# Kernel optimization log

Measured on AMD Instinct MI355X. Metric: run time of the kernel, lower is better.

Reference implementation:

```python
import jax, jax.numpy as jnp
import numpy as np

V = 32000   # vocab
H = 512     # hidden = embed dim
L = 2       # lstm layers
S = 64      # source length
K = 3       # beam width
T = 50      # max decode length
BOS = 1


def lstm_cell(x, h, c, Wih, Whh, b):
    # x,h,c: [B,H]; Wih/Whh: [4H,H]; b: [4H]
    z = x @ Wih.T + h @ Whh.T + b
    i, f, g, o = jnp.split(z, 4, axis=-1)
    c = jax.nn.sigmoid(f) * c + jax.nn.sigmoid(i) * jnp.tanh(g)
    h = jax.nn.sigmoid(o) * jnp.tanh(c)
    return h, c


def run_layer(x, Wih, Whh, b):
    # x: [S,B,H] -> outputs [S,B,H], final h,c [B,H]
    B = x.shape[1]
    z = jnp.zeros((B, H), x.dtype)
    def step(carry, xt):
        h, c = carry
        h, c = lstm_cell(xt, h, c, Wih, Whh, b)
        return (h, c), h
    (h, c), ys = jax.lax.scan(step, (z, z), x)
    return ys, h, c


def setup_inputs() -> dict:
    key = jax.random.key(0)
    ks = jax.random.split(key, 10)
    def p(k, shape, s=0.05):
        return jax.random.normal(k, shape, dtype=jnp.float32) * s
    return {
        'input_seq': jax.random.randint(ks[0], (S, 1), 0, V),
        'emb_enc': p(ks[1], (V, H), 0.1),
        'Wih_enc': p(ks[2], (L, 4 * H, H)),
        'Whh_enc': p(ks[3], (L, 4 * H, H)),
        'b_enc': jnp.zeros((L, 4 * H), jnp.float32),
        'emb_dec': p(ks[4], (V, H), 0.1),
        'Wih_dec': p(ks[5], (L, 4 * H, H)),
        'Whh_dec': p(ks[6], (L, 4 * H, H)),
        'b_dec': jnp.zeros((L, 4 * H), jnp.float32),
        'W_c': p(ks[7], (H, 2 * H)),
        'W_out': p(ks[8], (V, H)),
        'b_out': jnp.zeros((V,), jnp.float32),
        'input_length': S,
        'max_length': T,
        'bos': BOS,
    }


def reference(input_seq, emb_enc, Wih_enc, Whh_enc, b_enc,
              emb_dec, Wih_dec, Whh_dec, b_dec, W_c, W_out, b_out,
              input_length, max_length, bos):
    # ---- encoder ----
    x = emb_enc[input_seq[:, 0]][:, None, :]        # [S,1,H]
    hs, cs = [], []
    for l in range(L):
        x, hl, cl = run_layer(x, Wih_enc[l], Whh_enc[l], b_enc[l])
        hs.append(hl); cs.append(cl)
    enc_out = x[:, 0, :]                            # [S,H]
    h = jnp.stack(hs)                               # [L,1,H]
    c = jnp.stack(cs)

    # ---- decoder single step (vectorized over beam) ----
    def decode_step(tokens, h, c):
        x = emb_dec[tokens]                         # [B,H]
        nh, nc = [], []
        for l in range(L):
            hl, cl = lstm_cell(x, h[l], c[l], Wih_dec[l], Whh_dec[l], b_dec[l])
            nh.append(hl); nc.append(cl); x = hl
        attn = jax.nn.softmax(jnp.einsum('sh,bh->bs', enc_out, x), axis=-1)
        ctx = attn @ enc_out                        # [B,H]
        feat = jnp.tanh(jnp.concatenate([x, ctx], -1) @ W_c.T)
        probs = jax.nn.softmax(feat @ W_out.T + b_out)  # [B,V]
        return probs, jnp.stack(nh), jnp.stack(nc)

    # ---- first step (beam expand) ----
    probs, h, c = decode_step(jnp.array([bos]), h, c)
    topv, topi = jax.lax.top_k(probs[0], K)
    scores = jnp.log(topv)                          # [K]
    tokens = topi                                   # [K]
    h = jnp.repeat(h, K, axis=1)                    # [L,K,H]
    c = jnp.repeat(c, K, axis=1)
    backtrack = jnp.full((K, max_length), bos, dtype=jnp.int32)

    # ---- beam search loop ----
    def body(carry, t):
        tokens, h, c, scores, bt = carry
        probs, hn, cn = decode_step(tokens, h, c)   # [K,V]
        topv, topi = jax.lax.top_k(probs, K)        # [K,K]
        cum = jnp.log(topv) + scores[:, None]
        cand_scores, flat = jax.lax.top_k(cum.reshape(-1), K)
        best = topi.reshape(-1)[flat]
        orig = flat // K                            # beam origins
        bt = bt[orig].at[:, t + 1].set(tokens[orig])
        return (best, hn[:, orig, :], cn[:, orig, :], cand_scores, bt), None

    (tokens, h, c, scores, backtrack), _ = jax.lax.scan(
        body, (tokens, h, c, scores, backtrack), jnp.arange(max_length - 1))
    return backtrack[jnp.argmax(scores)]            # [max_length] tokens
```

## Files before the change

kernel.cpp:

```cpp
#include <hip/hip_runtime.h>
#include <math.h>

#define HSZ   512
#define H4    2048
#define SEQ   64
#define VOC   32000
#define BEAM  3
#define TMAX  50
#define FLS   16

#define LOFF  ((size_t)H4 * HSZ)

__device__ __forceinline__ float wsum(float v) {
#pragma unroll
  for (int off = 32; off; off >>= 1) v += __shfl_xor(v, off, 64);
  return v;
}
__device__ __forceinline__ float dot4(float4 a, float4 b) {
  return a.x * b.x + a.y * b.y + a.z * b.z + a.w * b.w;
}
__device__ __forceinline__ float sigf(float x) { return 1.f / (1.f + expf(-x)); }

__device__ __forceinline__ bool better(float v1, int i1, float v2, int i2) {
  return (v1 > v2) || (v1 == v2 && i1 < i2);
}
__device__ __forceinline__ void ins3(float* v, int* idx, float nv, int ni) {
  if (better(nv, ni, v[2], idx[2])) {
    if (better(nv, ni, v[1], idx[1])) {
      v[2] = v[1]; idx[2] = idx[1];
      if (better(nv, ni, v[0], idx[0])) { v[1] = v[0]; idx[1] = idx[0]; v[0] = nv; idx[0] = ni; }
      else { v[1] = nv; idx[1] = ni; }
    } else { v[2] = nv; idx[2] = ni; }
  }
}

__device__ __forceinline__ float agld(const float* p) {
  return __hip_atomic_load(p, __ATOMIC_RELAXED, __HIP_MEMORY_SCOPE_AGENT);
}
__device__ __forceinline__ void agst(float* p, float v) {
  __hip_atomic_store(p, v, __ATOMIC_RELAXED, __HIP_MEMORY_SCOPE_AGENT);
}
__device__ __forceinline__ int agldi(const int* p) {
  return __hip_atomic_load(p, __ATOMIC_RELAXED, __HIP_MEMORY_SCOPE_AGENT);
}


__global__ void __launch_bounds__(512) k_xw1(const float* __restrict__ Wih,
                                             const float* __restrict__ bias,
                                             const float* __restrict__ emb,
                                             const int* __restrict__ seq,
                                             float* __restrict__ xp1) {
  int t    = threadIdx.x & 63;
  int wave = threadIdx.x >> 6;
  int r    = blockIdx.x * 8 + wave;
  int tok  = seq[t];
  const float* xr = emb + (size_t)tok * HSZ;
  const float* wr = Wih + (size_t)r * HSZ;
  float acc = 0.f;
  for (int e = 0; e < HSZ; e += 4) {
    float4 wv = *(const float4*)(wr + e);
    float4 xv = *(const float4*)(xr + e);
    acc += dot4(wv, xv);
  }
  xp1[t * H4 + r] = acc + bias[r];
}

__global__ void __launch_bounds__(512) k_encslot(const float* __restrict__ Whh1,
                                                 const float* __restrict__ Wih2,
                                                 const float* __restrict__ Whh2,
                                                 const float* __restrict__ b2,
                                                 const float* __restrict__ xp1,
                                                 float* __restrict__ h1a, float* __restrict__ c1a,
                                                 float* __restrict__ h2a, float* __restrict__ c2a,
                                                 int s) {
  __shared__ float rowX[HSZ], rowH[HSZ], zl[16];
  int tid = threadIdx.x, wave = tid >> 6, lane = tid & 63;
  bool l2 = blockIdx.x >= 128;
  int t = l2 ? s - 1 : s;
  if (t < 0 || t >= SEQ) return;
  int bb = blockIdx.x & 127;
  int lr = wave >> 1;
  int j  = bb * 4 + lr;
  int g0 = (wave & 1) * 2;
  if (!l2) {
    rowX[tid] = (t > 0) ? h1a[t * HSZ + tid] : 0.f;
    __syncthreads();
    float4 h0 = ((const float4*)rowX)[lane], h1v = ((const float4*)rowX)[lane + 64];
#pragma unroll
    for (int gg = 0; gg < 2; ++gg) {
      int g = g0 + gg;
      int row = j + (g << 9);
      const float4* wr = (const float4*)(Whh1 + (size_t)row * HSZ);
      float zs = wsum(dot4(wr[lane], h0) + dot4(wr[lane + 64], h1v));
      if (lane == 0) zl[lr * 4 + g] = zs + xp1[t * H4 + row];
    }
    __syncthreads();
    if (tid < 4) {
      int j2 = bb * 4 + tid;
      float z0 = zl[tid * 4 + 0], z1 = zl[tid * 4 + 1], z2 = zl[tid * 4 + 2], z3 = zl[tid * 4 + 3];
      float cp = (t > 0) ? c1a[t * HSZ + j2] : 0.f;
      float c = sigf(z1) * cp + sigf(z0) * tanhf(z2);
      c1a[(t + 1) * HSZ + j2] = c;
      h1a[(t + 1) * HSZ + j2] = sigf(z3) * tanhf(c);
    }
  } else {
    rowX[tid] = h1a[(t + 1) * HSZ + tid];
    rowH[tid] = (t > 0) ? h2a[t * HSZ + tid] : 0.f;
    __syncthreads();
    float4 x0 = ((const float4*)rowX)[lane], x1 = ((const float4*)rowX)[lane + 64];
    float4 h0 = ((const float4*)rowH)[lane], h1v = ((const float4*)rowH)[lane + 64];
#pragma unroll
    for (int gg = 0; gg < 2; ++gg) {
      int g = g0 + gg;
      int row = j + (g << 9);
      const float4* wi = (const float4*)(Wih2 + (size_t)row * HSZ);
      const float4* wh = (const float4*)(Whh2 + (size_t)row * HSZ);
      float zs = wsum(dot4(wi[lane], x0) + dot4(wi[lane + 64], x1) +
                      dot4(wh[lane], h0) + dot4(wh[lane + 64], h1v));
      if (lane == 0) zl[lr * 4 + g] = zs + b2[row];
    }
    __syncthreads();
    if (tid < 4) {
      int j2 = bb * 4 + tid;
      float z0 = zl[tid * 4 + 0], z1 = zl[tid * 4 + 1], z2 = zl[tid * 4 + 2], z3 = zl[tid * 4 + 3];
      float cp = (t > 0) ? c2a[t * HSZ + j2] : 0.f;
      float c = sigf(z1) * cp + sigf(z0) * tanhf(z2);
      c2a[(t + 1) * HSZ + j2] = c;
      h2a[(t + 1) * HSZ + j2] = sigf(z3) * tanhf(c);
    }
  }
}


template <int B, int BIN, int MODE>
__global__ void __launch_bounds__(512) k_dcell1(
    const float* __restrict__ Wih, const float* __restrict__ Whh,
    const float* __restrict__ bias,
    const float* __restrict__ emb_dec, const int* __restrict__ bosp,
    const float* __restrict__ h1prev, const float* __restrict__ c1prev,
    const float* __restrict__ h2prev, const float* __restrict__ c2prev,
    const float* __restrict__ pm, const float* __restrict__ ps,
    const float* __restrict__ pv, const int* __restrict__ pi,
    float* __restrict__ hout, float* __restrict__ cout,
    float* __restrict__ hd2p, float* __restrict__ cd2p,
    const float* __restrict__ scores_rd, float* __restrict__ scores_wr,
    const int* __restrict__ tokens_rd, int* __restrict__ tokens_wr,
    int* __restrict__ bt, int ti) {
  __shared__ float xl[B * HSZ], hl[B * HSZ], cl[B * HSZ], zl[8 * B];
  __shared__ float sM[3], sS[3], sV[3][3], sScore[3];
  __shared__ int sI[3][3], sOrig[3], sTokNew[3], sTokOld[3];
  int tid = threadIdx.x, wave = tid >> 6, lane = tid & 63;

  if (MODE >= 1) {
    if (wave < BIN) {
      int b = wave;
      float lm4[4], ls4[4];
      float M = -INFINITY;
#pragma unroll
      for (int q = 0; q < 4; ++q) {
        int blk2 = lane + q * 64;
        lm4[q] = pm[blk2 * 3 + b]; ls4[q] = ps[blk2 * 3 + b];
        M = fmaxf(M, lm4[q]);
      }
#pragma unroll
      for (int off = 32; off; off >>= 1) M = fmaxf(M, __shfl_xor(M, off, 64));
      float S = 0.f;
#pragma unroll
      for (int q = 0; q < 4; ++q) S += ls4[q] * expf(lm4[q] - M);
      S = wsum(S);
      float bv[3] = {-INFINITY, -INFINITY, -INFINITY};
      int bi3[3]  = {0x7fffffff, 0x7fffffff, 0x7fffffff};
#pragma unroll
      for (int q = 0; q < 4; ++q) {
        int blk2 = lane + q * 64;
#pragma unroll
        for (int k = 0; k < 3; ++k)
          ins3(bv, bi3, pv[(blk2 * 3 + b) * 3 + k], pi[(blk2 * 3 + b) * 3 + k]);
      }
#pragma unroll
      for (int off = 32; off; off >>= 1) {
        float ov[3]; int oi[3];
#pragma unroll
        for (int k = 0; k < 3; ++k) { ov[k] = __shfl_xor(bv[k], off, 64); oi[k] = __shfl_xor(bi3[k], off, 64); }
#pragma unroll
        for (int k = 0; k < 3; ++k) ins3(bv, bi3, ov[k], oi[k]);
      }
      if (lane == 0) {
        sM[b] = M; sS[b] = S;
#pragma unroll
        for (int k = 0; k < 3; ++k) { sV[b][k] = bv[k]; sI[b][k] = bi3[k]; }
      }
    }
    __syncthreads();
    if (tid == 0) {
      if (MODE == 1) {
        float off0 = -sM[0] - logf(sS[0]);
        for (int k = 0; k < 3; ++k) {
          sScore[k] = sV[0][k] + off0;
          sTokNew[k] = sI[0][k]; sOrig[k] = 0; sTokOld[k] = 0;
        }
      } else {
        float osc[3];
        for (int b = 0; b < 3; ++b) { osc[b] = scores_rd[b]; sTokOld[b] = tokens_rd[b]; }
        float cum[9];
        for (int b = 0; b < 3; ++b) {
          float o = osc[b] - sM[b] - logf(sS[b]);
          for (int k = 0; k < 3; ++k) cum[b * 3 + k] = sV[b][k] + o;
        }
        bool used[9] = {false, false, false, false, false, false, false, false, false};
        for (int k = 0; k < 3; ++k) {
          int bf = 0; float bb = -INFINITY;
          for (int f = 0; f < 9; ++f)
            if (!used[f] && cum[f] > bb) { bb = cum[f]; bf = f; }
          used[bf] = true;
          sScore[k] = bb;
          int ob = bf / 3;
          sOrig[k] = ob;
          sTokNew[k] = sI[ob][bf - ob * 3];
        }
      }
    }
    __syncthreads();
  }

  if (MODE == 0) {
    int bos = bosp[0];
    for (int i = tid; i < B * HSZ; i += 512) {
      xl[i] = emb_dec[(size_t)bos * HSZ + i];
      hl[i] = h1prev[i]; cl[i] = c1prev[i];
    }
    if (blockIdx.x == 0) {
      for (int i = tid; i < B * HSZ; i += 512) { hd2p[i] = h2prev[i]; cd2p[i] = c2prev[i]; }
    }
  } else {
    for (int i = tid; i < B * HSZ; i += 512) {
      int b = i >> 9, e = i & 511;
      xl[i] = emb_dec[(size_t)sTokNew[b] * HSZ + e];
      hl[i] = h1prev[sOrig[b] * HSZ + e];
      cl[i] = c1prev[sOrig[b] * HSZ + e];
    }
    if (blockIdx.x == 0) {
      for (int i = tid; i < B * HSZ; i += 512) {
        int b = i >> 9, e = i & 511;
        hd2p[i] = h2prev[sOrig[b] * HSZ + e];
        cd2p[i] = c2prev[sOrig[b] * HSZ + e];
      }
      if (MODE == 1) {
        int bos = bosp[0];
        for (int idx = tid; idx < BEAM * TMAX; idx += 512) bt[idx] = bos;
      } else {
        const int* src = bt + (ti & 1) * (BEAM * TMAX);
        int* dst = bt + ((ti + 1) & 1) * (BEAM * TMAX);
        for (int idx = tid; idx < BEAM * TMAX; idx += 512) {
          int k = idx / TMAX, jj = idx % TMAX, o = sOrig[k];
          dst[idx] = (jj == ti + 1) ? sTokOld[o] : src[o * TMAX + jj];
        }
      }
      if (tid < 3) { scores_wr[tid] = sScore[tid]; tokens_wr[tid] = sTokNew[tid]; }
    }
  }
  __syncthreads();

  int lr = wave >> 2;
  int g  = wave & 3;
  int j  = blockIdx.x * 2 + lr;
  int row = j + (g << 9);
  const float4* wi = (const float4*)(Wih + (size_t)row * HSZ);
  const float4* wh = (const float4*)(Whh + (size_t)row * HSZ);
  float4 wi0 = wi[lane], wi1 = wi[lane + 64], wh0 = wh[lane], wh1 = wh[lane + 64];
  float bb = bias[row];
#pragma unroll
  for (int b = 0; b < B; ++b) {
    float4 xv0 = ((const float4*)(xl + b * HSZ))[lane];
    float4 xv1 = ((const float4*)(xl + b * HSZ))[lane + 64];
    float4 hv0 = ((const float4*)(hl + b * HSZ))[lane];
    float4 hv1 = ((const float4*)(hl + b * HSZ))[lane + 64];
    float acc = dot4(wi0, xv0) + dot4(wi1, xv1) + dot4(wh0, hv0) + dot4(wh1, hv1);
    float z = wsum(acc) + bb;
    if (lane == 0) zl[(lr * 4 + g) * B + b] = z;
  }
  __syncthreads();
  for (int q = tid; q < 2 * B; q += 512) {
    int lr2 = q / B, b = q % B;
    int j2 = blockIdx.x * 2 + lr2;
    float z0 = zl[(lr2 * 4 + 0) * B + b], z1 = zl[(lr2 * 4 + 1) * B + b];
    float z2 = zl[(lr2 * 4 + 2) * B + b], z3 = zl[(lr2 * 4 + 3) * B + b];
    float c = sigf(z1) * cl[b * HSZ + j2] + sigf(z0) * tanhf(z2);
    cout[b * HSZ + j2] = c;
    hout[b * HSZ + j2] = sigf(z3) * tanhf(c);
  }
}

template <int B>
__global__ void __launch_bounds__(512) k_dcell2(const float* __restrict__ Wih,
                                                const float* __restrict__ Whh,
                                                const float* __restrict__ bias,
                                                const float* __restrict__ x,
                                                const float* __restrict__ hin,
                                                const float* __restrict__ cin,
                                                float* __restrict__ hout, float* __restrict__ cout) {
  __shared__ float xl[B * HSZ], hl[B * HSZ], cl[B * HSZ], zl[8 * B];
  int tid = threadIdx.x;
  for (int i = tid; i < B * HSZ; i += 512) { xl[i] = x[i]; hl[i] = hin[i]; cl[i] = cin[i]; }
  __syncthreads();
  int wave = tid >> 6, lane = tid & 63;
  int lr = wave >> 2;
  int g  = wave & 3;
  int j  = blockIdx.x * 2 + lr;
  int row = j + (g << 9);
  const float4* wi = (const float4*)(Wih + (size_t)row * HSZ);
  const float4* wh = (const float4*)(Whh + (size_t)row * HSZ);
  float4 wi0 = wi[lane], wi1 = wi[lane + 64], wh0 = wh[lane], wh1 = wh[lane + 64];
  float bb = bias[row];
#pragma unroll
  for (int b = 0; b < B; ++b) {
    float4 xv0 = ((const float4*)(xl + b * HSZ))[lane];
    float4 xv1 = ((const float4*)(xl + b * HSZ))[lane + 64];
    float4 hv0 = ((const float4*)(hl + b * HSZ))[lane];
    float4 hv1 = ((const float4*)(hl + b * HSZ))[lane + 64];
    float acc = dot4(wi0, xv0) + dot4(wi1, xv1) + dot4(wh0, hv0) + dot4(wh1, hv1);
    float z = wsum(acc) + bb;
    if (lane == 0) zl[(lr * 4 + g) * B + b] = z;
  }
  __syncthreads();
  for (int q = tid; q < 2 * B; q += 512) {
    int lr2 = q / B, b = q % B;
    int j2 = blockIdx.x * 2 + lr2;
    float z0 = zl[(lr2 * 4 + 0) * B + b], z1 = zl[(lr2 * 4 + 1) * B + b];
    float z2 = zl[(lr2 * 4 + 2) * B + b], z3 = zl[(lr2 * 4 + 3) * B + b];
    float c = sigf(z1) * cl[b * HSZ + j2] + sigf(z0) * tanhf(z2);
    cout[b * HSZ + j2] = c;
    hout[b * HSZ + j2] = sigf(z3) * tanhf(c);
  }
}

template <int B>
__global__ void __launch_bounds__(512, 1) k_atlg(const float* __restrict__ h2,
                                                 const float* __restrict__ enc,
                                                 const float* __restrict__ Wc,
                                                 const float* __restrict__ Wout,
                                                 const float* __restrict__ bout,
                                                 float* __restrict__ feat,
                                                 float* __restrict__ pm, float* __restrict__ ps,
                                                 float* __restrict__ pv, int* __restrict__ pi,
                                                 int* __restrict__ cnt, int ep) {
  __shared__ float xs[BEAM * HSZ], at[BEAM * SEQ], xcs[BEAM * 1024];
  __shared__ float fst[BEAM * HSZ];
  int tid = threadIdx.x, wave = tid >> 6, lane = tid & 63;

  if (blockIdx.x < 64) {
    for (int i = tid; i < B * HSZ; i += 512) xs[i] = h2[i];
    __syncthreads();
    if (tid < B * SEQ) {
      int b = tid >> 6, s2 = tid & 63;
      const float* er = enc + (s2 + 1) * HSZ;
      const float* xb = xs + b * HSZ;
      float acc = 0.f;
      for (int e = 0; e < HSZ; e += 4) {
        float4 ev = *(const float4*)(er + e);
        acc += ev.x * xb[e] + ev.y * xb[e + 1] + ev.z * xb[e + 2] + ev.w * xb[e + 3];
      }
      at[tid] = acc;
    }
    __syncthreads();
    if (tid < B) {
      float m = -INFINITY;
      for (int s2 = 0; s2 < SEQ; ++s2) m = fmaxf(m, at[tid * SEQ + s2]);
      float s = 0.f;
      for (int s2 = 0; s2 < SEQ; ++s2) { float e = expf(at[tid * SEQ + s2] - m); at[tid * SEQ + s2] = e; s += e; }
      float inv = 1.f / s;
      for (int s2 = 0; s2 < SEQ; ++s2) at[tid * SEQ + s2] *= inv;
    }
    __syncthreads();
    if (tid < 128) {
      int h4 = tid * 4;
      float4 acc[B];
#pragma unroll
      for (int b = 0; b < B; ++b) acc[b] = make_float4(0.f, 0.f, 0.f, 0.f);
      for (int s2 = 0; s2 < SEQ; ++s2) {
        float4 ev = *(const float4*)(enc + (s2 + 1) * HSZ + h4);
#pragma unroll
        for (int b = 0; b < B; ++b) {
          float a = at[b * SEQ + s2];
          acc[b].x += a * ev.x; acc[b].y += a * ev.y; acc[b].z += a * ev.z; acc[b].w += a * ev.w;
        }
      }
#pragma unroll
      for (int b = 0; b < B; ++b) *(float4*)(xcs + b * 1024 + 512 + h4) = acc[b];
    }
    for (int i = tid; i < B * HSZ; i += 512) {
      int b = i >> 9, hcol = i & 511;
      xcs[b * 1024 + hcol] = xs[b * HSZ + hcol];
    }
    __syncthreads();
    int j = blockIdx.x * 8 + wave;
    const float4* w = (const float4*)(Wc + (size_t)j * 1024);
    float4 w0 = w[lane], w1 = w[lane + 64], w2 = w[lane + 128], w3 = w[lane + 192];
#pragma unroll
    for (int b = 0; b < B; ++b) {
      const float4* xb = (const float4*)(xcs + b * 1024);
      float acc = dot4(w0, xb[lane]) + dot4(w1, xb[lane + 64]) +
                  dot4(w2, xb[lane + 128]) + dot4(w3, xb[lane + 192]);
      acc = wsum(acc);
      if (lane == 0) agst(&feat[b * HSZ + j], tanhf(acc));
    }
    __syncthreads();
    if (tid == 0)
      __hip_atomic_fetch_add(cnt, 1, __ATOMIC_RELAXED, __HIP_MEMORY_SCOPE_AGENT);
  }

  if (tid == 0) {
    int target = ep * 64;
    long it = 0;
    while (agldi(cnt) < target && it < 50000000L) {
      __builtin_amdgcn_s_sleep(4);
      ++it;
    }
  }
  asm volatile("" ::: "memory");
  __syncthreads();

  for (int i = tid; i < B * HSZ; i += 512) fst[i] = agld(&feat[i]);
  __syncthreads();
  int gid = blockIdx.x * 8 + wave;
  float4 f0[B], f1[B];
#pragma unroll
  for (int b = 0; b < B; ++b) {
    f0[b] = ((const float4*)(fst + b * HSZ))[lane];
    f1[b] = ((const float4*)(fst + b * HSZ))[lane + 64];
  }
  float m[B], ss[B], tv[B][3];
  int tix[B][3];
#pragma unroll
  for (int b = 0; b < B; ++b) {
    m[b] = -INFINITY; ss[b] = 0.f;
#pragma unroll
    for (int k = 0; k < 3; ++k) { tv[b][k] = -INFINITY; tix[b][k] = 0x7fffffff; }
  }
  {
    float4 a0[16], a1[16]; float ab[16]; int vr[16];
#pragma unroll
    for (int u = 0; u < 16; ++u) {
      int v = gid + u * 2048;
      vr[u] = v;
      if (v < VOC) {
        const float4* wr = (const float4*)(Wout + (size_t)v * HSZ);
        a0[u] = wr[lane]; a1[u] = wr[lane + 64]; ab[u] = bout[v];
      } else {
        a0[u] = make_float4(0.f, 0.f, 0.f, 0.f); a1[u] = a0[u]; ab[u] = 0.f;
      }
    }
#pragma unroll
    for (int u = 0; u < 16; ++u) {
      if (vr[u] >= VOC) continue;
#pragma unroll
      for (int b = 0; b < B; ++b) {
        float acc = wsum(dot4(a0[u], f0[b]) + dot4(a1[u], f1[b])) + ab[u];
        float mo = m[b], mn = fmaxf(mo, acc);
        ss[b] = ss[b] * expf(mo - mn) + expf(acc - mn);
        m[b]  = mn;
        ins3(tv[b], tix[b], acc, vr[u]);
      }
    }
  }
  __shared__ float lm[8][3], lss[8][3], lv[8][3][3];
  __shared__ int li[8][3][3];
  if (lane == 0) {
#pragma unroll
    for (int b = 0; b < B; ++b) {
      lm[wave][b] = m[b]; lss[wave][b] = ss[b];
#pragma unroll
      for (int k = 0; k < 3; ++k) { lv[wave][b][k] = tv[b][k]; li[wave][b][k] = tix[b][k]; }
    }
  }
  __syncthreads();
  if (tid < B) {
    int b = tid;
    float M = -INFINITY;
#pragma unroll
    for (int w2 = 0; w2 < 8; ++w2) M = fmaxf(M, lm[w2][b]);
    float S = 0.f;
#pragma unroll
    for (int w2 = 0; w2 < 8; ++w2) S += lss[w2][b] * expf(lm[w2][b] - M);
    float bv[3] = {-INFINITY, -INFINITY, -INFINITY};
    int bi3[3]  = {0x7fffffff, 0x7fffffff, 0x7fffffff};
#pragma unroll
    for (int w2 = 0; w2 < 8; ++w2)
#pragma unroll
      for (int k = 0; k < 3; ++k) ins3(bv, bi3, lv[w2][b][k], li[w2][b][k]);
    int o = blockIdx.x * 3 + b;
    pm[o] = M; ps[o] = S;
#pragma unroll
    for (int k = 0; k < 3; ++k) { pv[o * 3 + k] = bv[k]; pi[o * 3 + k] = bi3[k]; }
  }
}

__global__ void __launch_bounds__(256) k_tail(const float* __restrict__ pm,
                                              const float* __restrict__ ps,
                                              const float* __restrict__ pv,
                                              const int* __restrict__ pi,
                                              const float* __restrict__ scores_rd,
                                              const int* __restrict__ tokens_rd,
                                              int* __restrict__ bt, int* __restrict__ outp) {
  const int ti = TMAX - 2;
  __shared__ float sM[3], sS[3], sV[3][3], sScore[3];
  __shared__ int sI[3][3], sOrig[3], sTokOld[3], sKstar;
  int tid = threadIdx.x, wave = tid >> 6, lane = tid & 63;
  if (wave < 3) {
    int b = wave;
    float lm4[4], ls4[4];
    float M = -INFINITY;
#pragma unroll
    for (int q = 0; q < 4; ++q) {
      int blk2 = lane + q * 64;
      lm4[q] = pm[blk2 * 3 + b]; ls4[q] = ps[blk2 * 3 + b];
      M = fmaxf(M, lm4[q]);
    }
#pragma unroll
    for (int off = 32; off; off >>= 1) M = fmaxf(M, __shfl_xor(M, off, 64));
    float S = 0.f;
#pragma unroll
    for (int q = 0; q < 4; ++q) S += ls4[q] * expf(lm4[q] - M);
    S = wsum(S);
    float bv[3] = {-INFINITY, -INFINITY, -INFINITY};
    int bi3[3]  = {0x7fffffff, 0x7fffffff, 0x7fffffff};
#pragma unroll
    for (int q = 0; q < 4; ++q) {
      int blk2 = lane + q * 64;
#pragma unroll
      for (int k = 0; k < 3; ++k)
        ins3(bv, bi3, pv[(blk2 * 3 + b) * 3 + k], pi[(blk2 * 3 + b) * 3 + k]);
    }
#pragma unroll
    for (int off = 32; off; off >>= 1) {
      float ov[3]; int oi[3];
#pragma unroll
      for (int k = 0; k < 3; ++k) { ov[k] = __shfl_xor(bv[k], off, 64); oi[k] = __shfl_xor(bi3[k], off, 64); }
#pragma unroll
      for (int k = 0; k < 3; ++k) ins3(bv, bi3, ov[k], oi[k]);
    }
    if (lane == 0) {
      sM[b] = M; sS[b] = S;
#pragma unroll
      for (int k = 0; k < 3; ++k) { sV[b][k] = bv[k]; sI[b][k] = bi3[k]; }
    }
  }
  __syncthreads();
  if (tid == 0) {
    float osc[3];
    for (int b = 0; b < 3; ++b) { osc[b] = scores_rd[b]; sTokOld[b] = tokens_rd[b]; }
    float cum[9];
    for (int b = 0; b < 3; ++b) {
      float o = osc[b] - sM[b] - logf(sS[b]);
      for (int k = 0; k < 3; ++k) cum[b * 3 + k] = sV[b][k] + o;
    }
    bool used[9] = {false, false, false, false, false, false, false, false, false};
    for (int k = 0; k < 3; ++k) {
      int bf = 0; float bb = -INFINITY;
      for (int f = 0; f < 9; ++f)
        if (!used[f] && cum[f] > bb) { bb = cum[f]; bf = f; }
      used[bf] = true;
      sScore[k] = bb;
      sOrig[k] = bf / 3;
    }
    float bb = -INFINITY; int kk = 0;
    for (int k = 0; k < 3; ++k) if (sScore[k] > bb) { bb = sScore[k]; kk = k; }
    sKstar = kk;
  }
  __syncthreads();
  const int* src = bt + (ti & 1) * (BEAM * TMAX);
  int* dst = bt + ((ti + 1) & 1) * (BEAM * TMAX);
  for (int idx = tid; idx < BEAM * TMAX; idx += 256) {
    int k = idx / TMAX, jj = idx % TMAX, o = sOrig[k];
    dst[idx] = (jj == ti + 1) ? sTokOld[o] : src[o * TMAX + jj];
  }
  __syncthreads();
  for (int jj = tid; jj < TMAX; jj += 256) outp[jj] = dst[sKstar * TMAX + jj];
}

extern "C" void kernel_launch(void* const* d_in, const int* in_sizes, int n_in,
                              void* d_out, int out_size, void* d_ws, size_t ws_size,
                              hipStream_t stream) {
  const int*   seq     = (const int*)d_in[0];
  const float* emb_enc = (const float*)d_in[1];
  const float* Wih_enc = (const float*)d_in[2];
  const float* Whh_enc = (const float*)d_in[3];
  const float* b_enc   = (const float*)d_in[4];
  const float* emb_dec = (const float*)d_in[5];
  const float* Wih_dec = (const float*)d_in[6];
  const float* Whh_dec = (const float*)d_in[7];
  const float* b_dec   = (const float*)d_in[8];
  const float* W_c     = (const float*)d_in[9];
  const float* W_out   = (const float*)d_in[10];
  const float* b_out   = (const float*)d_in[11];
  const int*   bosp    = (const int*)d_in[14];

  int* cnt = (int*)d_ws;
  float* w = (float*)d_ws + FLS;
  float* xp1     = w; w += SEQ * H4;
  float* h1a     = w; w += (SEQ + 1) * HSZ;
  float* c1a     = w; w += (SEQ + 1) * HSZ;
  float* h2a     = w; w += (SEQ + 1) * HSZ;
  float* c2a     = w; w += (SEQ + 1) * HSZ;
  float* hdn1    = w; w += 2 * BEAM * HSZ;
  float* cdn1    = w; w += 2 * BEAM * HSZ;
  float* hdn2    = w; w += 2 * BEAM * HSZ;
  float* cdn2    = w; w += 2 * BEAM * HSZ;
  float* hd2p    = w; w += BEAM * HSZ;
  float* cd2p    = w; w += BEAM * HSZ;
  float* feat    = w; w += BEAM * HSZ;
  float* pm      = w; w += 256 * 3;
  float* ps      = w; w += 256 * 3;
  float* pv      = w; w += 256 * 3 * 3;
  float* sb      = w; w += 2 * 4;
  int* pi     = (int*)w; w += 256 * 3 * 3;
  int* tb     = (int*)w; w += 2 * 4;
  int* bt     = (int*)w; w += 2 * BEAM * TMAX + 4;
  int* outp   = (int*)d_out;

  hipMemsetAsync(cnt, 0, FLS * sizeof(int), stream);

  k_xw1<<<256, 512, 0, stream>>>(Wih_enc, b_enc, emb_enc, seq, xp1);
  for (int s = 0; s <= SEQ; ++s)
    k_encslot<<<256, 512, 0, stream>>>(Whh_enc, Wih_enc + LOFF, Whh_enc + LOFF, b_enc + H4,
                                       xp1, h1a, c1a, h2a, c2a, s);

  for (int s = 0; s < TMAX; ++s) {
    int rp = (s - 1) & 1, wp = s & 1;
    if (s == 0) {
      k_dcell1<1, 1, 0><<<256, 512, 0, stream>>>(
          Wih_dec, Whh_dec, b_dec, emb_dec, bosp,
          h1a + SEQ * HSZ, c1a + SEQ * HSZ, h2a + SEQ * HSZ, c2a + SEQ * HSZ,
          pm, ps, pv, pi,
          hdn1 + 0, cdn1 + 0, hd2p, cd2p,
          sb, sb, tb, tb, bt, 0);
      k_dcell2<1><<<256, 512, 0, stream>>>(Wih_dec + LOFF, Whh_dec + LOFF, b_dec + H4,
                                           hdn1 + 0, hd2p, cd2p, hdn2 + 0, cdn2 + 0);
      k_atlg<1><<<256, 512, 0, stream>>>(hdn2 + 0, h2a, W_c, W_out, b_out, feat,
                                         pm, ps, pv, pi, cnt, s + 1);
    } else {
      float* h1p = hdn1 + rp * BEAM * HSZ; float* c1p = cdn1 + rp * BEAM * HSZ;
      float* h2p = hdn2 + rp * BEAM * HSZ; float* c2p = cdn2 + rp * BEAM * HSZ;
      float* h1o = hdn1 + wp * BEAM * HSZ; float* c1o = cdn1 + wp * BEAM * HSZ;
      float* h2o = hdn2 + wp * BEAM * HSZ; float* c2o = cdn2 + wp * BEAM * HSZ;
      if (s == 1)
        k_dcell1<3, 1, 1><<<256, 512, 0, stream>>>(
            Wih_dec, Whh_dec, b_dec, emb_dec, bosp,
            h1p, c1p, h2p, c2p, pm, ps, pv, pi,
            h1o, c1o, hd2p, cd2p,
            sb + rp * 4, sb + wp * 4, tb + rp * 4, tb + wp * 4, bt, -1);
      else
        k_dcell1<3, 3, 2><<<256, 512, 0, stream>>>(
            Wih_dec, Whh_dec, b_dec, emb_dec, bosp,
            h1p, c1p, h2p, c2p, pm, ps, pv, pi,
            h1o, c1o, hd2p, cd2p,
            sb + rp * 4, sb + wp * 4, tb + rp * 4, tb + wp * 4, bt, s - 2);
      k_dcell2<3><<<256, 512, 0, stream>>>(Wih_dec + LOFF, Whh_dec + LOFF, b_dec + H4,
                                           h1o, hd2p, cd2p, h2o, c2o);
      k_atlg<3><<<256, 512, 0, stream>>>(h2o, h2a, W_c, W_out, b_out, feat,
                                         pm, ps, pv, pi, cnt, s + 1);
    }
  }
  k_tail<<<1, 256, 0, stream>>>(pm, ps, pv, pi, sb + 4, tb + 4, bt, outp);
}
```

Before: 3.775 ms.

## Remap output-projection GEMV to four threads per vocab row with shuffle merge

Replaces the wave-per-row output-logit loop (16 rows per wave, full-wave reductions per row and beam) with a layout where each group of four threads computes one vocab row over a quarter of the hidden dimension. Per-row online softmax state and top-3 are then merged with a cross-lane shuffle tree. Zero-sum guards are added to the softmax merges so empty lanes (m=-inf, s=0) do not produce NaN. It also drops the min-blocks-per-SM launch-bounds hint. The goal is to cut the many per-row wave reductions and sequential exp updates, at the cost of strided per-thread loads and a longer merge tree.

```diff
diff --git a/kernel.cpp b/kernel.cpp
--- a/kernel.cpp
+++ b/kernel.cpp
@@ -166,7 +166,7 @@
       for (int off = 32; off; off >>= 1) M = fmaxf(M, __shfl_xor(M, off, 64));
       float S = 0.f;
 #pragma unroll
-      for (int q = 0; q < 4; ++q) S += ls4[q] * expf(lm4[q] - M);
+      for (int q = 0; q < 4; ++q) S += (ls4[q] == 0.f) ? 0.f : ls4[q] * expf(lm4[q] - M);
       S = wsum(S);
       float bv[3] = {-INFINITY, -INFINITY, -INFINITY};
       int bi3[3]  = {0x7fffffff, 0x7fffffff, 0x7fffffff};
@@ -335,15 +335,15 @@
 }
 
 template <int B>
-__global__ void __launch_bounds__(512, 1) k_atlg(const float* __restrict__ h2,
-                                                 const float* __restrict__ enc,
-                                                 const float* __restrict__ Wc,
-                                                 const float* __restrict__ Wout,
-                                                 const float* __restrict__ bout,
-                                                 float* __restrict__ feat,
-                                                 float* __restrict__ pm, float* __restrict__ ps,
-                                                 float* __restrict__ pv, int* __restrict__ pi,
-                                                 int* __restrict__ cnt, int ep) {
+__global__ void __launch_bounds__(512) k_atlg2(const float* __restrict__ h2,
+                                               const float* __restrict__ enc,
+                                               const float* __restrict__ Wc,
+                                               const float* __restrict__ Wout,
+                                               const float* __restrict__ bout,
+                                               float* __restrict__ feat,
+                                               float* __restrict__ pm, float* __restrict__ ps,
+                                               float* __restrict__ pv, int* __restrict__ pi,
+                                               int* __restrict__ cnt, int ep) {
   __shared__ float xs[BEAM * HSZ], at[BEAM * SEQ], xcs[BEAM * 1024];
   __shared__ float fst[BEAM * HSZ];
   int tid = threadIdx.x, wave = tid >> 6, lane = tid & 63;
@@ -412,23 +412,17 @@
   if (tid == 0) {
     int target = ep * 64;
     long it = 0;
-    while (agldi(cnt) < target && it < 50000000L) {
-      __builtin_amdgcn_s_sleep(4);
-      ++it;
-    }
+    while (agldi(cnt) < target && it < 50000000L) { __builtin_amdgcn_s_sleep(4); ++it; }
   }
   asm volatile("" ::: "memory");
   __syncthreads();
 
   for (int i = tid; i < B * HSZ; i += 512) fst[i] = agld(&feat[i]);
   __syncthreads();
-  int gid = blockIdx.x * 8 + wave;
-  float4 f0[B], f1[B];
-#pragma unroll
-  for (int b = 0; b < B; ++b) {
-    f0[b] = ((const float4*)(fst + b * HSZ))[lane];
-    f1[b] = ((const float4*)(fst + b * HSZ))[lane + 64];
-  }
+
+  int gq   = blockIdx.x * 512 + tid;
+  int grow = gq >> 2;
+  int qtr  = tid & 3;
   float m[B], ss[B], tv[B][3];
   int tix[B][3];
 #pragma unroll
@@ -437,30 +431,51 @@
 #pragma unroll
     for (int k = 0; k < 3; ++k) { tv[b][k] = -INFINITY; tix[b][k] = 0x7fffffff; }
   }
-  {
-    float4 a0[16], a1[16]; float ab[16]; int vr[16];
-#pragma unroll
-    for (int u = 0; u < 16; ++u) {
-      int v = gid + u * 2048;
-      vr[u] = v;
-      if (v < VOC) {
-        const float4* wr = (const float4*)(Wout + (size_t)v * HSZ);
-        a0[u] = wr[lane]; a1[u] = wr[lane + 64]; ab[u] = bout[v];
-      } else {
-        a0[u] = make_float4(0.f, 0.f, 0.f, 0.f); a1[u] = a0[u]; ab[u] = 0.f;
-      }
-    }
-#pragma unroll
-    for (int u = 0; u < 16; ++u) {
-      if (vr[u] >= VOC) continue;
-#pragma unroll
-      for (int b = 0; b < B; ++b) {
-        float acc = wsum(dot4(a0[u], f0[b]) + dot4(a1[u], f1[b])) + ab[u];
-        float mo = m[b], mn = fmaxf(mo, acc);
-        ss[b] = ss[b] * expf(mo - mn) + expf(acc - mn);
-        m[b]  = mn;
-        ins3(tv[b], tix[b], acc, vr[u]);
-      }
+  if (grow < VOC) {
+    const float4* wr = (const float4*)(Wout + (size_t)grow * HSZ) + qtr * 32;
+    const float4* f4[B];
+#pragma unroll
+    for (int b = 0; b < B; ++b) f4[b] = ((const float4*)(fst + b * HSZ)) + qtr * 32;
+    float acc[B];
+#pragma unroll
+    for (int b = 0; b < B; ++b) acc[b] = 0.f;
+#pragma unroll
+    for (int e0 = 0; e0 < 32; e0 += 8) {
+      float4 wv[8];
+#pragma unroll
+      for (int u = 0; u < 8; ++u) wv[u] = wr[e0 + u];
+#pragma unroll
+      for (int u = 0; u < 8; ++u)
+#pragma unroll
+        for (int b = 0; b < B; ++b) acc[b] += dot4(wv[u], f4[b][e0 + u]);
+    }
+    float bo = bout[grow];
+#pragma unroll
+    for (int b = 0; b < B; ++b) {
+      float t = acc[b];
+      t += __shfl_xor(t, 1, 64);
+      t += __shfl_xor(t, 2, 64);
+      if (qtr == 0) {
+        float logit = t + bo;
+        m[b] = logit; ss[b] = 1.f; tv[b][0] = logit; tix[b][0] = grow;
+      }
+    }
+  }
+#pragma unroll
+  for (int off = 32; off; off >>= 1) {
+#pragma unroll
+    for (int b = 0; b < B; ++b) {
+      float Mo = __shfl_xor(m[b], off, 64);
+      float So = __shfl_xor(ss[b], off, 64);
+      float ov[3]; int oi[3];
+#pragma unroll
+      for (int k = 0; k < 3; ++k) { ov[k] = __shfl_xor(tv[b][k], off, 64); oi[k] = __shfl_xor(tix[b][k], off, 64); }
+      float Mn = fmaxf(m[b], Mo);
+      float t1 = (ss[b] == 0.f) ? 0.f : ss[b] * expf(m[b] - Mn);
+      float t2 = (So == 0.f) ? 0.f : So * expf(Mo - Mn);
+      m[b] = Mn; ss[b] = t1 + t2;
+#pragma unroll
+      for (int k = 0; k < 3; ++k) ins3(tv[b], tix[b], ov[k], oi[k]);
     }
   }
   __shared__ float lm[8][3], lss[8][3], lv[8][3][3];
@@ -481,7 +496,8 @@
     for (int w2 = 0; w2 < 8; ++w2) M = fmaxf(M, lm[w2][b]);
     float S = 0.f;
 #pragma unroll
-    for (int w2 = 0; w2 < 8; ++w2) S += lss[w2][b] * expf(lm[w2][b] - M);
+    for (int w2 = 0; w2 < 8; ++w2)
+      S += (lss[w2][b] == 0.f) ? 0.f : lss[w2][b] * expf(lm[w2][b] - M);
     float bv[3] = {-INFINITY, -INFINITY, -INFINITY};
     int bi3[3]  = {0x7fffffff, 0x7fffffff, 0x7fffffff};
 #pragma unroll
@@ -520,7 +536,7 @@
     for (int off = 32; off; off >>= 1) M = fmaxf(M, __shfl_xor(M, off, 64));
     float S = 0.f;
 #pragma unroll
-    for (int q = 0; q < 4; ++q) S += ls4[q] * expf(lm4[q] - M);
+    for (int q = 0; q < 4; ++q) S += (ls4[q] == 0.f) ? 0.f : ls4[q] * expf(lm4[q] - M);
     S = wsum(S);
     float bv[3] = {-INFINITY, -INFINITY, -INFINITY};
     int bi3[3]  = {0x7fffffff, 0x7fffffff, 0x7fffffff};
@@ -636,8 +652,8 @@
           sb, sb, tb, tb, bt, 0);
       k_dcell2<1><<<256, 512, 0, stream>>>(Wih_dec + LOFF, Whh_dec + LOFF, b_dec + H4,
                                            hdn1 + 0, hd2p, cd2p, hdn2 + 0, cdn2 + 0);
-      k_atlg<1><<<256, 512, 0, stream>>>(hdn2 + 0, h2a, W_c, W_out, b_out, feat,
-                                         pm, ps, pv, pi, cnt, s + 1);
+      k_atlg2<1><<<256, 512, 0, stream>>>(hdn2 + 0, h2a, W_c, W_out, b_out, feat,
+                                          pm, ps, pv, pi, cnt, s + 1);
     } else {
       float* h1p = hdn1 + rp * BEAM * HSZ; float* c1p = cdn1 + rp * BEAM * HSZ;
       float* h2p = hdn2 + rp * BEAM * HSZ; float* c2p = cdn2 + rp * BEAM * HSZ;
@@ -657,8 +673,8 @@
             sb + rp * 4, sb + wp * 4, tb + rp * 4, tb + wp * 4, bt, s - 2);
       k_dcell2<3><<<256, 512, 0, stream>>>(Wih_dec + LOFF, Whh_dec + LOFF, b_dec + H4,
                                            h1o, hd2p, cd2p, h2o, c2o);
-      k_atlg<3><<<256, 512, 0, stream>>>(h2o, h2a, W_c, W_out, b_out, feat,
-                                         pm, ps, pv, pi, cnt, s + 1);
+      k_atlg2<3><<<256, 512, 0, stream>>>(h2o, h2a, W_c, W_out, b_out, feat,
+                                          pm, ps, pv, pi, cnt, s + 1);
     }
   }
   k_tail<<<1, 256, 0, stream>>>(pm, ps, pv, pi, sb + 4, tb + 4, bt, outp);
```

New measurement: 4.916 ms. 30.2% more time.

## Stage W_out rows through shared-memory tiles in logits kernel with contiguous row blocks

Applied to the files above, without the earlier changes.

The vocab projection now gives each of 250 blocks a contiguous 128-row slice of W_out. The slice is loaded in 16-row tiles through a 32 KB shared buffer with fully coalesced float4 loads, replacing the old scheme of 16 strided rows held in registers per wave. Blocks 250-255 do no logits work and report empty partials. Zero-sum guards were added in the softmax merges so these empty partials (-inf max) do not produce NaN. The change aims to improve load coalescing and register pressure, but it drops the memory-level parallelism of 16 in-flight row loads and adds two block barriers per tile, and the extra LDS may lower occupancy.

```diff
diff --git a/kernel.cpp b/kernel.cpp
--- a/kernel.cpp
+++ b/kernel.cpp
@@ -166,7 +166,7 @@
       for (int off = 32; off; off >>= 1) M = fmaxf(M, __shfl_xor(M, off, 64));
       float S = 0.f;
 #pragma unroll
-      for (int q = 0; q < 4; ++q) S += ls4[q] * expf(lm4[q] - M);
+      for (int q = 0; q < 4; ++q) S += (ls4[q] == 0.f) ? 0.f : ls4[q] * expf(lm4[q] - M);
       S = wsum(S);
       float bv[3] = {-INFINITY, -INFINITY, -INFINITY};
       int bi3[3]  = {0x7fffffff, 0x7fffffff, 0x7fffffff};
@@ -335,17 +335,18 @@
 }
 
 template <int B>
-__global__ void __launch_bounds__(512, 1) k_atlg(const float* __restrict__ h2,
-                                                 const float* __restrict__ enc,
-                                                 const float* __restrict__ Wc,
-                                                 const float* __restrict__ Wout,
-                                                 const float* __restrict__ bout,
-                                                 float* __restrict__ feat,
-                                                 float* __restrict__ pm, float* __restrict__ ps,
-                                                 float* __restrict__ pv, int* __restrict__ pi,
-                                                 int* __restrict__ cnt, int ep) {
+__global__ void __launch_bounds__(512) k_atlg3(const float* __restrict__ h2,
+                                               const float* __restrict__ enc,
+                                               const float* __restrict__ Wc,
+                                               const float* __restrict__ Wout,
+                                               const float* __restrict__ bout,
+                                               float* __restrict__ feat,
+                                               float* __restrict__ pm, float* __restrict__ ps,
+                                               float* __restrict__ pv, int* __restrict__ pi,
+                                               int* __restrict__ cnt, int ep) {
   __shared__ float xs[BEAM * HSZ], at[BEAM * SEQ], xcs[BEAM * 1024];
   __shared__ float fst[BEAM * HSZ];
+  __shared__ float tile[16 * HSZ];
   int tid = threadIdx.x, wave = tid >> 6, lane = tid & 63;
 
   if (blockIdx.x < 64) {
@@ -412,17 +413,14 @@
   if (tid == 0) {
     int target = ep * 64;
     long it = 0;
-    while (agldi(cnt) < target && it < 50000000L) {
-      __builtin_amdgcn_s_sleep(4);
-      ++it;
-    }
+    while (agldi(cnt) < target && it < 50000000L) { __builtin_amdgcn_s_sleep(4); ++it; }
   }
   asm volatile("" ::: "memory");
   __syncthreads();
 
   for (int i = tid; i < B * HSZ; i += 512) fst[i] = agld(&feat[i]);
   __syncthreads();
-  int gid = blockIdx.x * 8 + wave;
+
   float4 f0[B], f1[B];
 #pragma unroll
   for (int b = 0; b < B; ++b) {
@@ -437,32 +435,41 @@
 #pragma unroll
     for (int k = 0; k < 3; ++k) { tv[b][k] = -INFINITY; tix[b][k] = 0x7fffffff; }
   }
-  {
-    float4 a0[16], a1[16]; float ab[16]; int vr[16];
-#pragma unroll
-    for (int u = 0; u < 16; ++u) {
-      int v = gid + u * 2048;
-      vr[u] = v;
-      if (v < VOC) {
-        const float4* wr = (const float4*)(Wout + (size_t)v * HSZ);
-        a0[u] = wr[lane]; a1[u] = wr[lane + 64]; ab[u] = bout[v];
-      } else {
-        a0[u] = make_float4(0.f, 0.f, 0.f, 0.f); a1[u] = a0[u]; ab[u] = 0.f;
-      }
-    }
-#pragma unroll
-    for (int u = 0; u < 16; ++u) {
-      if (vr[u] >= VOC) continue;
-#pragma unroll
-      for (int b = 0; b < B; ++b) {
-        float acc = wsum(dot4(a0[u], f0[b]) + dot4(a1[u], f1[b])) + ab[u];
-        float mo = m[b], mn = fmaxf(mo, acc);
-        ss[b] = ss[b] * expf(mo - mn) + expf(acc - mn);
-        m[b]  = mn;
-        ins3(tv[b], tix[b], acc, vr[u]);
-      }
-    }
-  }
+
+  if (blockIdx.x < 250) {
+    int row0 = blockIdx.x * 128;
+#pragma unroll 1
+    for (int t = 0; t < 8; ++t) {
+      const float4* gsrc = (const float4*)(Wout + (size_t)(row0 + t * 16) * HSZ);
+      float4 stg0 = gsrc[0 * 512 + tid];
+      float4 stg1 = gsrc[1 * 512 + tid];
+      float4 stg2 = gsrc[2 * 512 + tid];
+      float4 stg3 = gsrc[3 * 512 + tid];
+      __syncthreads();
+      ((float4*)tile)[0 * 512 + tid] = stg0;
+      ((float4*)tile)[1 * 512 + tid] = stg1;
+      ((float4*)tile)[2 * 512 + tid] = stg2;
+      ((float4*)tile)[3 * 512 + tid] = stg3;
+      __syncthreads();
+#pragma unroll
+      for (int rr = 0; rr < 2; ++rr) {
+        int rl  = wave * 2 + rr;
+        int row = row0 + t * 16 + rl;
+        const float4* wr = (const float4*)(tile + rl * HSZ);
+        float4 w0 = wr[lane], w1 = wr[lane + 64];
+        float bo = bout[row];
+#pragma unroll
+        for (int b = 0; b < B; ++b) {
+          float acc = wsum(dot4(w0, f0[b]) + dot4(w1, f1[b])) + bo;
+          float mo = m[b], mn = fmaxf(mo, acc);
+          ss[b] = (ss[b] == 0.f) ? expf(acc - mn) : ss[b] * expf(mo - mn) + expf(acc - mn);
+          m[b]  = mn;
+          ins3(tv[b], tix[b], acc, row);
+        }
+      }
+    }
+  }
+
   __shared__ float lm[8][3], lss[8][3], lv[8][3][3];
   __shared__ int li[8][3][3];
   if (lane == 0) {
@@ -481,7 +488,8 @@
     for (int w2 = 0; w2 < 8; ++w2) M = fmaxf(M, lm[w2][b]);
     float S = 0.f;
 #pragma unroll
-    for (int w2 = 0; w2 < 8; ++w2) S += lss[w2][b] * expf(lm[w2][b] - M);
+    for (int w2 = 0; w2 < 8; ++w2)
+      S += (lss[w2][b] == 0.f) ? 0.f : lss[w2][b] * expf(lm[w2][b] - M);
     float bv[3] = {-INFINITY, -INFINITY, -INFINITY};
     int bi3[3]  = {0x7fffffff, 0x7fffffff, 0x7fffffff};
 #pragma unroll
@@ -520,7 +528,7 @@
     for (int off = 32; off; off >>= 1) M = fmaxf(M, __shfl_xor(M, off, 64));
     float S = 0.f;
 #pragma unroll
-    for (int q = 0; q < 4; ++q) S += ls4[q] * expf(lm4[q] - M);
+    for (int q = 0; q < 4; ++q) S += (ls4[q] == 0.f) ? 0.f : ls4[q] * expf(lm4[q] - M);
     S = wsum(S);
     float bv[3] = {-INFINITY, -INFINITY, -INFINITY};
     int bi3[3]  = {0x7fffffff, 0x7fffffff, 0x7fffffff};
@@ -636,8 +644,8 @@
           sb, sb, tb, tb, bt, 0);
       k_dcell2<1><<<256, 512, 0, stream>>>(Wih_dec + LOFF, Whh_dec + LOFF, b_dec + H4,
                                            hdn1 + 0, hd2p, cd2p, hdn2 + 0, cdn2 + 0);
-      k_atlg<1><<<256, 512, 0, stream>>>(hdn2 + 0, h2a, W_c, W_out, b_out, feat,
-                                         pm, ps, pv, pi, cnt, s + 1);
+      k_atlg3<1><<<256, 512, 0, stream>>>(hdn2 + 0, h2a, W_c, W_out, b_out, feat,
+                                          pm, ps, pv, pi, cnt, s + 1);
     } else {
       float* h1p = hdn1 + rp * BEAM * HSZ; float* c1p = cdn1 + rp * BEAM * HSZ;
       float* h2p = hdn2 + rp * BEAM * HSZ; float* c2p = cdn2 + rp * BEAM * HSZ;
@@ -657,8 +665,8 @@
             sb + rp * 4, sb + wp * 4, tb + rp * 4, tb + wp * 4, bt, s - 2);
       k_dcell2<3><<<256, 512, 0, stream>>>(Wih_dec + LOFF, Whh_dec + LOFF, b_dec + H4,
                                            h1o, hd2p, cd2p, h2o, c2o);
-      k_atlg<3><<<256, 512, 0, stream>>>(h2o, h2a, W_c, W_out, b_out, feat,
-                                         pm, ps, pv, pi, cnt, s + 1);
+      k_atlg3<3><<<256, 512, 0, stream>>>(h2o, h2a, W_c, W_out, b_out, feat,
+                                          pm, ps, pv, pi, cnt, s + 1);
     }
   }
   k_tail<<<1, 256, 0, stream>>>(pm, ps, pv, pi, sb + 4, tb + 4, bt, outp);
```

New measurement: 3.761 ms. No clear change (-0.4%).
